# Optimization experiments

Hardware: AMD Instinct MI355X
Metric: run time of the kernel (lower is better)

Reference implementation:

```python
import jax, jax.numpy as jnp
import numpy as np

B, N, C = 4, 2304, 256
H = 8                      # num_heads
D = C // H                 # head_dim = 32
SCALE = D ** -0.5
H_DS, W_DS = 48, 48
UP = 2                     # spatial_down_ratio
EPS = 1e-5


def setup_inputs() -> dict:
    key = jax.random.key(0)
    ks = jax.random.split(key, 16)
    g = lambda k, shape, s: (jax.random.normal(k, shape, dtype=jnp.float32) * s)
    return {
        "x1": g(ks[0], (B, N, C), 1.0),
        "x2": g(ks[1], (B, N, C), 1.0),
        # attention projections (torch Linear convention: [out, in], no bias)
        "q1_w": g(ks[2], (C, C), C ** -0.5),
        "kv1_w": g(ks[3], (2 * C, C), C ** -0.5),
        "q2_w": g(ks[4], (C, C), C ** -0.5),
        "kv2_w": g(ks[5], (2 * C, C), C ** -0.5),
        # per-head scalar biases
        "beta12": jnp.full((H,), 0.2, dtype=jnp.float32),
        "beta21": jnp.full((H,), 0.1, dtype=jnp.float32),
        # output projections
        "p1_w": g(ks[6], (C, C), (2.0 / C) ** 0.5),
        "p1_b": g(ks[7], (C,), 1e-2),
        "p2_w": g(ks[8], (C, C), (2.0 / C) ** 0.5),
        "p2_b": g(ks[9], (C,), 1e-2),
        # LayerNorm affine params
        "g1": jnp.ones((C,), dtype=jnp.float32),
        "b1": jnp.zeros((C,), dtype=jnp.float32),
        "g2": jnp.ones((C,), dtype=jnp.float32),
        "b2": jnp.zeros((C,), dtype=jnp.float32),
    }


def _heads(x):
    # [B,N,C] -> [B,H,N,D]
    return x.reshape(B, N, H, D).transpose(0, 2, 1, 3)


def _merge(x):
    # [B,H,N,D] -> [B,N,C]
    return x.transpose(0, 2, 1, 3).reshape(B, N, C)


def _cross_attn(q, k, v, beta):
    # scores: [B,H,N,N] with per-head scalar bias
    s = jnp.einsum("bhqd,bhkd->bhqk", q, k) * SCALE + beta[None, :, None, None]
    a = jax.nn.softmax(s, axis=-1)
    return jnp.einsum("bhqk,bhkd->bhqd", a, v)


def _layernorm(x, g, b):
    mu = jnp.mean(x, axis=-1, keepdims=True)
    var = jnp.var(x, axis=-1, keepdims=True)
    return (x - mu) * jax.lax.rsqrt(var + EPS) * g + b


def _forward(x1, x2, q1_w, kv1_w, q2_w, kv2_w, beta12, beta21,
             p1_w, p1_b, p2_w, p2_b, g1, b1, g2, b2):
    q1 = _heads(x1 @ q1_w.T)
    kv1 = x1 @ kv1_w.T          # [B,N,2C]
    k1, v1 = _heads(kv1[..., :C]), _heads(kv1[..., C:])
    q2 = _heads(x2 @ q2_w.T)
    kv2 = x2 @ kv2_w.T
    k2, v2 = _heads(kv2[..., :C]), _heads(kv2[..., C:])

    o1 = _merge(_cross_attn(q1, k2, v2, beta12))   # x1 attends to x2
    o2 = _merge(_cross_attn(q2, k1, v1, beta21))   # x2 attends to x1

    y1 = _layernorm(jax.nn.relu(o1 @ p1_w.T + p1_b), g1, b1)
    y2 = _layernorm(jax.nn.relu(o2 @ p2_w.T + p2_b), g2, b2)

    # [B,N,C] -> [B,C,H_ds,W_ds]
    y1 = y1.transpose(0, 2, 1).reshape(B, C, H_DS, W_DS)
    y2 = y2.transpose(0, 2, 1).reshape(B, C, H_DS, W_DS)

    # bilinear upsample x2, align_corners=False (half-pixel == jax.image default)
    out_shape = (B, C, H_DS * UP, W_DS * UP)
    y1 = jax.image.resize(y1, out_shape, method="bilinear")
    y2 = jax.image.resize(y2, out_shape, method="bilinear")
    return y1, y2


def reference(x1, x2, q1_w, kv1_w, q2_w, kv2_w, beta12, beta21,
              p1_w, p1_b, p2_w, p2_b, g1, b1, g2, b2):
    return _forward(x1, x2, q1_w, kv1_w, q2_w, kv2_w, beta12, beta21,
                    p1_w, p1_b, p2_w, p2_b, g1, b1, g2, b2)
```

## Files before the change

kernel.cpp:

```cpp
#include <hip/hip_runtime.h>
#include <math.h>


typedef __attribute__((ext_vector_type(8))) short short8;
typedef __attribute__((ext_vector_type(4))) float f32x4;
typedef __attribute__((ext_vector_type(16))) float f32x16;
typedef __attribute__((ext_vector_type(2))) unsigned uint32x2;

#define MFMA16(a, b, c) __builtin_amdgcn_mfma_f32_16x16x32_bf16((a), (b), (c), 0, 0, 0)
#define MFMA32(a, b, c) __builtin_amdgcn_mfma_f32_32x32x16_bf16((a), (b), (c), 0, 0, 0)

__device__ __forceinline__ float bf2f(ushort u) {
    union { unsigned u; float f; } x; x.u = ((unsigned)u) << 16; return x.f;
}
__device__ __forceinline__ ushort f2bf(float f) {
    union { float f; unsigned u; } x; x.f = f;
    unsigned u = x.u;
    return (ushort)((u + 0x7fffu + ((u >> 16) & 1u)) >> 16);
}
__device__ __forceinline__ unsigned cvt_pk_bf16(float a, float b) {
    unsigned r;
    asm("v_cvt_pk_bf16_f32 %0, %1, %2" : "=v"(r) : "v"(a), "v"(b));
    return r;
}
__device__ __forceinline__ float fast_ex2(float x) {
    float r;
    asm("v_exp_f32 %0, %1" : "=v"(r) : "v"(x));
    return r;
}
__device__ __forceinline__ void plswap(unsigned &a, unsigned &b) {
    uint32x2 r = __builtin_amdgcn_permlane32_swap(a, b, false, false);
    a = r[0]; b = r[1];
}

__global__ void sniff_kernel(const ushort* __restrict__ x, int* __restrict__ flag)
{
    int lane = threadIdx.x;
    ushort u = x[lane * 2];
    int e = (u >> 7) & 0xFF;
    int outlier = (e < 100 || e > 135) ? 1 : 0;
    unsigned long long m = __ballot(outlier);
    if (lane == 0) *flag = (__popcll(m) >= 16) ? 1 : 0;
}

__global__ __launch_bounds__(256) void convert_params(
    const void* s0, const void* s1, const void* s2, const void* s3,
    const void* s4, const void* s5, const void* s6, const void* s7,
    const void* s8, const void* s9, const void* s10, const void* s11,
    ushort* __restrict__ dst, const int* __restrict__ flag)
{
    int idx = blockIdx.x * 256 + threadIdx.x;
    if (idx >= 525824) return;
    const void* src; int off;
    if      (idx < 65536)  { src = s0;  off = idx; }
    else if (idx < 196608) { src = s1;  off = idx - 65536; }
    else if (idx < 262144) { src = s2;  off = idx - 196608; }
    else if (idx < 393216) { src = s3;  off = idx - 262144; }
    else if (idx < 458752) { src = s4;  off = idx - 393216; }
    else if (idx < 524288) { src = s5;  off = idx - 458752; }
    else if (idx < 524544) { src = s6;  off = idx - 524288; }
    else if (idx < 524800) { src = s7;  off = idx - 524544; }
    else if (idx < 525056) { src = s8;  off = idx - 524800; }
    else if (idx < 525312) { src = s9;  off = idx - 525056; }
    else if (idx < 525568) { src = s10; off = idx - 525312; }
    else                   { src = s11; off = idx - 525568; }
    ushort v = (*flag) ? f2bf(((const float*)src)[off])
                       : ((const ushort*)src)[off];
    dst[idx] = v;
}

__global__ __launch_bounds__(256) void convert_x(
    const void* __restrict__ x1, const void* __restrict__ x2,
    ushort* __restrict__ o1, ushort* __restrict__ o2,
    const int* __restrict__ flag)
{
    int idx = blockIdx.x * 256 + threadIdx.x;
    int which = idx >= 294912;
    int off = (which ? idx - 294912 : idx) * 8;
    const void* src = which ? x2 : x1;
    ushort* dst = which ? o2 : o1;
    if (*flag) {
        const float* p = (const float*)src + off;
        float4 a = *(const float4*)p;
        float4 c = *(const float4*)(p + 4);
        uint4 u;
        u.x = cvt_pk_bf16(a.x, a.y);
        u.y = cvt_pk_bf16(a.z, a.w);
        u.z = cvt_pk_bf16(c.x, c.y);
        u.w = cvt_pk_bf16(c.z, c.w);
        *(uint4*)(dst + off) = u;
    } else {
        *(uint4*)(dst + off) = *(const uint4*)((const ushort*)src + off);
    }
}

__global__ __launch_bounds__(256) void gemm_bt(
    const void* __restrict__ Ain, const ushort* __restrict__ W,
    ushort* __restrict__ C, const ushort* __restrict__ bias,
    int M, int N, int K, int relu, const int* __restrict__ dflag, int a_ext,
    int mode, ushort* __restrict__ Kh, ushort* __restrict__ Vt,
    const ushort* __restrict__ W2, const ushort* __restrict__ bias2,
    ushort* __restrict__ Kh2, ushort* __restrict__ Vt2, int mhalf)
{
    __shared__ __align__(16) ushort As[128][40];
    __shared__ __align__(16) ushort Ws[128][40];

    const int m0 = blockIdx.x * 128;
    const int n0 = blockIdx.y * 128;
    const int tid = threadIdx.x;
    const int w = tid >> 6;
    const int wr = w >> 1, wc = w & 1;
    const int lane = tid & 63;
    const int lm = lane & 15;
    const int quad = lane >> 4;
    const int a32 = a_ext ? *dflag : 0;

    const int side = (mhalf && m0 >= mhalf) ? 1 : 0;
    const ushort* Wu = side ? W2 : W;
    const ushort* bu = side ? bias2 : bias;
    ushort* Khu = side ? Kh2 : Kh;
    ushort* Vtu = side ? Vt2 : Vt;

    const f32x4 Z4 = {0.f, 0.f, 0.f, 0.f};
    f32x4 acc[4][4];
    for (int i = 0; i < 4; i++)
        for (int j = 0; j < 4; j++) acc[i][j] = Z4;

    const ushort* A16 = (const ushort*)Ain;
    const float*  A32 = (const float*)Ain;
    const int row = tid >> 1, off16 = (tid & 1) * 16;

    for (int k0 = 0; k0 < K; k0 += 32) {
        __syncthreads();
        if (a32) {
            const float* p0 = A32 + (size_t)(m0 + row) * K + k0 + off16;
            float4 f0 = *(const float4*)p0;
            float4 f1 = *(const float4*)(p0 + 4);
            float4 f2 = *(const float4*)(p0 + 8);
            float4 f3 = *(const float4*)(p0 + 12);
            uint4 t0, t1;
            t0.x = cvt_pk_bf16(f0.x, f0.y);
            t0.y = cvt_pk_bf16(f0.z, f0.w);
            t0.z = cvt_pk_bf16(f1.x, f1.y);
            t0.w = cvt_pk_bf16(f1.z, f1.w);
            t1.x = cvt_pk_bf16(f2.x, f2.y);
            t1.y = cvt_pk_bf16(f2.z, f2.w);
            t1.z = cvt_pk_bf16(f3.x, f3.y);
            t1.w = cvt_pk_bf16(f3.z, f3.w);
            *(uint4*)&As[row][off16]     = t0;
            *(uint4*)&As[row][off16 + 8] = t1;
        } else {
            const ushort* p0 = A16 + (size_t)(m0 + row) * K + k0 + off16;
            *(uint4*)&As[row][off16]     = *(const uint4*)p0;
            *(uint4*)&As[row][off16 + 8] = *(const uint4*)(p0 + 8);
        }
        {
            const ushort* p0 = Wu + (size_t)(n0 + row) * K + k0 + off16;
            *(uint4*)&Ws[row][off16]     = *(const uint4*)p0;
            *(uint4*)&Ws[row][off16 + 8] = *(const uint4*)(p0 + 8);
        }
        __syncthreads();

        short8 af[4], wf[4];
        #pragma unroll
        for (int mt = 0; mt < 4; mt++)
            af[mt] = *(const short8*)&As[wr * 64 + mt * 16 + lm][quad * 8];
        #pragma unroll
        for (int nt = 0; nt < 4; nt++)
            wf[nt] = *(const short8*)&Ws[wc * 64 + nt * 16 + lm][quad * 8];
        #pragma unroll
        for (int mt = 0; mt < 4; mt++)
            #pragma unroll
            for (int nt = 0; nt < 4; nt++)
                acc[mt][nt] = MFMA16(af[mt], wf[nt], acc[mt][nt]);
    }

    if (mode == 1) {
        const float QSC = 0.17677669529663687f * 1.4426950408889634f;
        #pragma unroll
        for (int mt = 0; mt < 4; mt++) {
            const int grow = m0 + wr * 64 + mt * 16 + quad * 4;
            const int grel = grow - (side ? mhalf : 0);
            int bb = grel / 2304;
            int tok = grel - bb * 2304;
            #pragma unroll
            for (int nt = 0; nt < 4; nt++) {
                int col = n0 + wc * 64 + nt * 16 + lm;
                if (col < 256) {
                    for (int r = 0; r < 4; r++)
                        C[(size_t)(grow + r) * 256 + col] = f2bf(acc[mt][nt][r] * QSC);
                } else if (col < 512) {
                    int c2 = col - 256, hh = c2 >> 5, d = c2 & 31;
                    size_t kb = ((size_t)(bb * 8 + hh) * 72 + (tok >> 5)) * 1024
                              + (size_t)(d >> 4) * 512 + (size_t)(d & 15);
                    for (int r = 0; r < 4; r++)
                        Khu[kb + (size_t)((tok + r) & 31) * 16] = f2bf(acc[mt][nt][r]);
                } else {
                    int c2 = col - 512, hh = c2 >> 5, d = c2 & 31;
                    size_t vb = ((size_t)(bb * 8 + hh) * 144 + (tok >> 4)) * 512
                              + (size_t)d * 16 + (size_t)(tok & 15);
                    uint2 o;
                    o.x = cvt_pk_bf16(acc[mt][nt][0], acc[mt][nt][1]);
                    o.y = cvt_pk_bf16(acc[mt][nt][2], acc[mt][nt][3]);
                    *(uint2*)&Vtu[vb] = o;
                }
            }
        }
    } else {
        #pragma unroll
        for (int mt = 0; mt < 4; mt++) {
            const int grow = m0 + wr * 64 + mt * 16 + quad * 4;
            #pragma unroll
            for (int nt = 0; nt < 4; nt++) {
                int col = n0 + wc * 64 + nt * 16 + lm;
                float bv = bu ? bf2f(bu[col]) : 0.f;
                for (int r = 0; r < 4; r++) {
                    float v = acc[mt][nt][r] + bv;
                    if (relu) v = fmaxf(v, 0.f);
                    C[(size_t)(grow + r) * N + col] = f2bf(v);
                }
            }
        }
    }
}

__global__ __launch_bounds__(256) void attn_kernel(
    const ushort* __restrict__ Qa, const ushort* __restrict__ Kha,
    const ushort* __restrict__ Vta, ushort* __restrict__ Oa,
    const ushort* __restrict__ Qb, const ushort* __restrict__ Khb2,
    const ushort* __restrict__ Vtb2, ushort* __restrict__ Ob)
{
    __shared__ float Lo[4][2][64][16];
    __shared__ float Ll[4][2][64];

    const int sid = blockIdx.x;
    const int qb = blockIdx.y;
    const int side = sid >> 5;
    const int bh = sid & 31;
    const ushort* Q  = side ? Qb   : Qa;
    const ushort* Kh = side ? Khb2 : Kha;
    const ushort* Vt = side ? Vtb2 : Vta;
    ushort* O        = side ? Ob   : Oa;

    const int b = bh >> 3, h = bh & 7;
    const int tid = threadIdx.x;
    const int w = tid >> 6, lane = tid & 63;
    const int l31 = lane & 31, hl = lane >> 5;

    const int qrow0 = qb * 64 + l31;
    const int qrow1 = qrow0 + 32;
    const ushort* qp0 = Q + ((size_t)b * 2304 + qrow0) * 256 + h * 32 + hl * 8;
    const ushort* qp1 = Q + ((size_t)b * 2304 + qrow1) * 256 + h * 32 + hl * 8;
    const short8 qf0a = *(const short8*)qp0;
    const short8 qf1a = *(const short8*)(qp0 + 16);
    const short8 qf0b = *(const short8*)qp1;
    const short8 qf1b = *(const short8*)(qp1 + 16);

    f32x16 oa, ob;
    #pragma unroll
    for (int i = 0; i < 16; i++) { oa[i] = 0.f; ob[i] = 0.f; }
    const f32x16 Z16 = oa;
    float la = 0.f, lb = 0.f;

    const ushort* kp0 = Kh + (size_t)bh * 73728 + l31 * 16 + hl * 8;
    const ushort* vp0 = Vt + (size_t)bh * 73728 + l31 * 16 + hl * 8;

#define LOADT(kf0v, kf1v, vf0v, vf1v, t) { \
    const ushort* _kp = kp0 + (size_t)(t) * 1024; \
    kf0v = *(const short8*)_kp; \
    kf1v = *(const short8*)(_kp + 512); \
    const ushort* _vp = vp0 + (size_t)(t) * 1024; \
    vf0v = *(const short8*)_vp; \
    vf1v = *(const short8*)(_vp + 512); \
}
#define QSET(kf0v, kf1v, vf0v, vf1v, qf0v, qf1v, oacc, lacc) { \
    f32x16 s = MFMA32(kf0v, qf0v, Z16); \
    s = MFMA32(kf1v, qf1v, s); \
    float p[16]; \
    _Pragma("unroll") \
    for (int i = 0; i < 16; i++) p[i] = fast_ex2(s[i]); \
    lacc += (((p[0] + p[1]) + (p[2] + p[3])) + ((p[4] + p[5]) + (p[6] + p[7]))) \
          + (((p[8] + p[9]) + (p[10] + p[11])) + ((p[12] + p[13]) + (p[14] + p[15]))); \
    unsigned c0 = cvt_pk_bf16(p[0],  p[1]); \
    unsigned c1 = cvt_pk_bf16(p[2],  p[3]); \
    unsigned c2 = cvt_pk_bf16(p[4],  p[5]); \
    unsigned c3 = cvt_pk_bf16(p[6],  p[7]); \
    unsigned c4 = cvt_pk_bf16(p[8],  p[9]); \
    unsigned c5 = cvt_pk_bf16(p[10], p[11]); \
    unsigned c6 = cvt_pk_bf16(p[12], p[13]); \
    unsigned c7 = cvt_pk_bf16(p[14], p[15]); \
    plswap(c0, c2); plswap(c1, c3); plswap(c4, c6); plswap(c5, c7); \
    union { unsigned u[4]; short8 s8; } pA, pB; \
    pA.u[0] = c0; pA.u[1] = c1; pA.u[2] = c2; pA.u[3] = c3; \
    pB.u[0] = c4; pB.u[1] = c5; pB.u[2] = c6; pB.u[3] = c7; \
    oacc = MFMA32(vf0v, pA.s8, oacc); \
    oacc = MFMA32(vf1v, pB.s8, oacc); \
}
#define COMP(kf0v, kf1v, vf0v, vf1v) { \
    QSET(kf0v, kf1v, vf0v, vf1v, qf0a, qf1a, oa, la); \
    QSET(kf0v, kf1v, vf0v, vf1v, qf0b, qf1b, ob, lb); \
}

    short8 kA0, kA1, vA0, vA1;
    short8 kB0, kB1, vB0, vB1;

    const int t0 = w * 18;

    LOADT(kA0, kA1, vA0, vA1, t0);
    LOADT(kB0, kB1, vB0, vB1, t0 + 1);

    for (int i = 0; i < 9; i++) {
        COMP(kA0, kA1, vA0, vA1);
        { int ta = t0 + 2 * i + 2; ta = ta < 72 ? ta : 70;
          LOADT(kA0, kA1, vA0, vA1, ta); }
        COMP(kB0, kB1, vB0, vB1);
        { int tb = t0 + 2 * i + 3; tb = tb < 72 ? tb : 71;
          LOADT(kB0, kB1, vB0, vB1, tb); }
    }
#undef LOADT
#undef QSET
#undef COMP

    la += __shfl_xor(la, 32, 64);
    lb += __shfl_xor(lb, 32, 64);

    #pragma unroll
    for (int r = 0; r < 16; r++) {
        Lo[w][0][lane][r] = oa[r];
        Lo[w][1][lane][r] = ob[r];
    }
    Ll[w][0][lane] = la;
    Ll[w][1][lane] = lb;
    __syncthreads();

    if (w < 2) {
        float os[16];
        #pragma unroll
        for (int r = 0; r < 16; r++) os[r] = 0.f;
        float ls = 0.f;
        #pragma unroll
        for (int u = 0; u < 4; u++) {
            ls += Ll[u][w][lane];
            #pragma unroll
            for (int r = 0; r < 16; r++) os[r] += Lo[u][w][lane][r];
        }
        float rl = 1.f / ls;
        const int qrow = (w == 0) ? qrow0 : qrow1;
        ushort* op = O + ((size_t)b * 2304 + qrow) * 256 + h * 32 + hl * 4;
        #pragma unroll
        for (int g = 0; g < 4; g++) {
            uint2 o;
            o.x = cvt_pk_bf16(os[4 * g] * rl, os[4 * g + 1] * rl);
            o.y = cvt_pk_bf16(os[4 * g + 2] * rl, os[4 * g + 3] * rl);
            *(uint2*)(op + 8 * g) = o;
        }
    }
}

__global__ __launch_bounds__(256) void lnt_kernel(
    const ushort* __restrict__ Z, const ushort* __restrict__ G1,
    const ushort* __restrict__ B1, const ushort* __restrict__ G2,
    const ushort* __restrict__ B2, ushort* __restrict__ Yt)
{
    __shared__ ushort T[256][72];

    const int tid = threadIdx.x;
    const int tok0 = blockIdx.x * 32;
    const int half = (tok0 >= 9216) ? 1 : 0;
    const int tr = tok0 - half * 9216;
    const int bb = tr / 2304;
    const int tokb = tr - bb * 2304;

    const int tok_l = tid >> 3;
    const int cq = tid & 7;

    const ushort* zp = Z + ((size_t)(tok0 + tok_l)) * 256 + cq * 32;
    uint dd[16];
    for (int i = 0; i < 4; i++) {
        uint4 v = *(const uint4*)(zp + i * 8);
        dd[i * 4 + 0] = v.x; dd[i * 4 + 1] = v.y;
        dd[i * 4 + 2] = v.z; dd[i * 4 + 3] = v.w;
    }
    float s = 0.f, q = 0.f;
    for (int e = 0; e < 16; e++) {
        float x0 = bf2f((ushort)dd[e]);
        float x1 = bf2f((ushort)(dd[e] >> 16));
        s += x0 + x1;
        q += x0 * x0 + x1 * x1;
    }
    s += __shfl_xor(s, 1, 64); q += __shfl_xor(q, 1, 64);
    s += __shfl_xor(s, 2, 64); q += __shfl_xor(q, 2, 64);
    s += __shfl_xor(s, 4, 64); q += __shfl_xor(q, 4, 64);
    float mu = s * (1.f / 256.f);
    float var = q * (1.f / 256.f) - mu * mu;
    float rs = rsqrtf(var + 1e-5f);

    const ushort* Gs = half ? G2 : G1;
    const ushort* Bs = half ? B2 : B1;
    const int col = tok_l + 4 * cq;

    for (int i = 0; i < 4; i++) {
        int cb = cq * 32 + i * 8;
        uint4 gv = *(const uint4*)(Gs + cb);
        uint4 bv = *(const uint4*)(Bs + cb);
        uint gg[4] = {gv.x, gv.y, gv.z, gv.w};
        uint bw[4] = {bv.x, bv.y, bv.z, bv.w};
        for (int k = 0; k < 4; k++) {
            uint u = dd[i * 4 + k];
            float x0 = bf2f((ushort)u), x1 = bf2f((ushort)(u >> 16));
            float y0 = (x0 - mu) * rs * bf2f((ushort)gg[k]) + bf2f((ushort)bw[k]);
            float y1 = (x1 - mu) * rs * bf2f((ushort)(gg[k] >> 16))
                     + bf2f((ushort)(bw[k] >> 16));
            int c = cb + 2 * k;
            T[c][col]     = f2bf(y0);
            T[c + 1][col] = f2bf(y1);
        }
    }
    __syncthreads();

    const int c_row = tid >> 3;
    const int tq = (tid & 7) * 4;
    const size_t obase = ((size_t)((half * 4 + bb) * 256)) * 2304 + tokb + tq;
    for (int i = 0; i < 8; i++) {
        int c = c_row + 32 * i;
        uint2 v = *(const uint2*)&T[c][tq + 4 * i];
        *(uint2*)(Yt + obase + (size_t)c * 2304) = v;
    }
}

__global__ __launch_bounds__(256) void upsample_kernel(
    const ushort* __restrict__ Yt, float* __restrict__ out)
{
    int idx = blockIdx.x * 256 + threadIdx.x;
    int m  = idx % 48;
    int t  = idx / 48;
    int oi = t % 96;
    int bc = t / 96;

    float fi = oi * 0.5f - 0.25f;
    int i0 = (int)floorf(fi);
    float wi = fi - (float)i0;
    int i1 = i0 + 1 < 47 ? i0 + 1 : 47;
    i0 = i0 > 0 ? i0 : 0;
    int jm = m - 1 > 0 ? m - 1 : 0;
    int jp = m + 1 < 47 ? m + 1 : 47;

    const ushort* r0 = Yt + (size_t)bc * 2304 + i0 * 48;
    const ushort* r1 = Yt + (size_t)bc * 2304 + i1 * 48;
    float a0 = bf2f(r0[jm]), b0 = bf2f(r0[m]), c0 = bf2f(r0[jp]);
    float a1 = bf2f(r1[jm]), b1 = bf2f(r1[m]), c1 = bf2f(r1[jp]);
    float u = 1.f - wi;
    float ha = u * a0 + wi * a1;
    float hb = u * b0 + wi * b1;
    float hc = u * c0 + wi * c1;
    float2 o;
    o.x = 0.25f * ha + 0.75f * hb;
    o.y = 0.75f * hb + 0.25f * hc;
    *(float2*)(out + (size_t)bc * 9216 + oi * 96 + m * 2) = o;
}

extern "C" void kernel_launch(void* const* d_in, const int* in_sizes, int n_in,
                              void* d_out, int out_size, void* d_ws, size_t ws_size,
                              hipStream_t stream)
{
    (void)in_sizes; (void)n_in; (void)out_size; (void)ws_size;

    ushort* ws  = (ushort*)d_ws;
    ushort* Q1  = ws;
    ushort* Q2  = Q1  + 2359296;
    ushort* KV1 = Q2  + 2359296;
    ushort* KV2 = KV1 + 4718592;
    ushort* wc  = KV2 + 4718592;
    int*    dflag = (int*)(wc + 525824);

    ushort* cqkv1w = wc;
    ushort* cqkv2w = wc + 196608;
    ushort* cp1w  = wc + 393216;
    ushort* cp2w  = wc + 458752;
    ushort* cp1b  = wc + 524288;
    ushort* cp2b  = wc + 524544;
    ushort* cg1   = wc + 524800;
    ushort* cb1   = wc + 525056;
    ushort* cg2   = wc + 525312;
    ushort* cb2   = wc + 525568;

    float*  outf = (float*)d_out;
    ushort* O1  = (ushort*)d_out;
    ushort* O2  = O1 + 2359296;
    ushort* Xb1 = O2 + 2359296;
    ushort* Xb2 = Xb1 + 2359296;
    ushort* Z1  = KV2;
    ushort* Yt  = Q1;
    (void)Q2; (void)O2; (void)Xb2;

    dim3 blk(256);
    sniff_kernel<<<dim3(1), dim3(64), 0, stream>>>((const ushort*)d_in[0], dflag);
    convert_params<<<dim3(2054), blk, 0, stream>>>(
        d_in[2], d_in[3], d_in[4], d_in[5], d_in[8], d_in[10],
        d_in[9], d_in[11], d_in[12], d_in[13], d_in[14], d_in[15],
        wc, dflag);
    convert_x<<<dim3(2304), blk, 0, stream>>>(d_in[0], d_in[1], Xb1, Xb2, dflag);

    gemm_bt<<<dim3(144, 6), blk, 0, stream>>>(Xb1, cqkv1w, Q1, nullptr,
        18432, 768, 256, 0, dflag, 0, 1, KV1, KV1 + 2359296,
        cqkv2w, nullptr, KV2, KV2 + 2359296, 9216);

    attn_kernel<<<dim3(64, 36), dim3(256), 0, stream>>>(
        Q1, KV2, KV2 + 2359296, O1,
        Q2, KV1, KV1 + 2359296, O2);

    gemm_bt<<<dim3(144, 2), blk, 0, stream>>>(O1, cp1w, Z1, cp1b,
        18432, 256, 256, 1, dflag, 0, 0, nullptr, nullptr,
        cp2w, cp2b, nullptr, nullptr, 9216);

    lnt_kernel<<<dim3(576), blk, 0, stream>>>(Z1, cg1, cb1, cg2, cb2, Yt);

    upsample_kernel<<<dim3(36864), blk, 0, stream>>>(Yt, outf);
}
```

Baseline: 249.6 us.

## Fuse output projection with LayerNorm-transpose and merge prep kernels

Replaces the separate output-projection GEMM and the LayerNorm/transpose kernel with a single kernel that computes 64 full-width rows per block, applies bias+ReLU, reduces row statistics across waves via shared memory, normalizes, and writes the transposed layout directly. It also merges the dtype-sniff, parameter conversion and input conversion into one launch, with every block recomputing the sniff flag. The aim is to remove the intermediate Z round trip through global memory and several launch overheads. In exchange the fused GEMM uses fewer blocks (288) with unpipelined loads, and the dflag passed to gemm_bt becomes null.

```diff
diff --git a/kernel.cpp b/kernel.cpp
--- a/kernel.cpp
+++ b/kernel.cpp
@@ -33,64 +33,61 @@
     a = r[0]; b = r[1];
 }
 
-__global__ void sniff_kernel(const ushort* __restrict__ x, int* __restrict__ flag)
-{
-    int lane = threadIdx.x;
-    ushort u = x[lane * 2];
-    int e = (u >> 7) & 0xFF;
-    int outlier = (e < 100 || e > 135) ? 1 : 0;
-    unsigned long long m = __ballot(outlier);
-    if (lane == 0) *flag = (__popcll(m) >= 16) ? 1 : 0;
-}
-
-__global__ __launch_bounds__(256) void convert_params(
+__global__ __launch_bounds__(256) void prep_kernel(
+    const void* __restrict__ x1, const void* __restrict__ x2,
+    ushort* __restrict__ xo1, ushort* __restrict__ xo2,
     const void* s0, const void* s1, const void* s2, const void* s3,
     const void* s4, const void* s5, const void* s6, const void* s7,
     const void* s8, const void* s9, const void* s10, const void* s11,
-    ushort* __restrict__ dst, const int* __restrict__ flag)
+    ushort* __restrict__ dst)
 {
-    int idx = blockIdx.x * 256 + threadIdx.x;
-    if (idx >= 525824) return;
-    const void* src; int off;
-    if      (idx < 65536)  { src = s0;  off = idx; }
-    else if (idx < 196608) { src = s1;  off = idx - 65536; }
-    else if (idx < 262144) { src = s2;  off = idx - 196608; }
-    else if (idx < 393216) { src = s3;  off = idx - 262144; }
-    else if (idx < 458752) { src = s4;  off = idx - 393216; }
-    else if (idx < 524288) { src = s5;  off = idx - 458752; }
-    else if (idx < 524544) { src = s6;  off = idx - 524288; }
-    else if (idx < 524800) { src = s7;  off = idx - 524544; }
-    else if (idx < 525056) { src = s8;  off = idx - 524800; }
-    else if (idx < 525312) { src = s9;  off = idx - 525056; }
-    else if (idx < 525568) { src = s10; off = idx - 525312; }
-    else                   { src = s11; off = idx - 525568; }
-    ushort v = (*flag) ? f2bf(((const float*)src)[off])
-                       : ((const ushort*)src)[off];
-    dst[idx] = v;
-}
-
-__global__ __launch_bounds__(256) void convert_x(
-    const void* __restrict__ x1, const void* __restrict__ x2,
-    ushort* __restrict__ o1, ushort* __restrict__ o2,
-    const int* __restrict__ flag)
-{
-    int idx = blockIdx.x * 256 + threadIdx.x;
-    int which = idx >= 294912;
-    int off = (which ? idx - 294912 : idx) * 8;
-    const void* src = which ? x2 : x1;
-    ushort* dst = which ? o2 : o1;
-    if (*flag) {
-        const float* p = (const float*)src + off;
-        float4 a = *(const float4*)p;
-        float4 c = *(const float4*)(p + 4);
-        uint4 u;
-        u.x = cvt_pk_bf16(a.x, a.y);
-        u.y = cvt_pk_bf16(a.z, a.w);
-        u.z = cvt_pk_bf16(c.x, c.y);
-        u.w = cvt_pk_bf16(c.z, c.w);
-        *(uint4*)(dst + off) = u;
-    } else {
-        *(uint4*)(dst + off) = *(const uint4*)((const ushort*)src + off);
+    {
+        ushort u = ((const ushort*)x1)[(threadIdx.x & 63) * 2];
+        int e = (u >> 7) & 0xFF;
+        int outlier = (e < 100 || e > 135) ? 1 : 0;
+        unsigned long long mk = __ballot(outlier);
+        int flag = (__popcll(mk) >= 16) ? 1 : 0;
+
+        int bid = blockIdx.x;
+        if (bid < 2304) {
+            int idx = bid * 256 + threadIdx.x;
+            int which = idx >= 294912;
+            int off = (which ? idx - 294912 : idx) * 8;
+            const void* src = which ? x2 : x1;
+            ushort* o = which ? xo2 : xo1;
+            if (flag) {
+                const float* p = (const float*)src + off;
+                float4 a = *(const float4*)p;
+                float4 c = *(const float4*)(p + 4);
+                uint4 u4;
+                u4.x = cvt_pk_bf16(a.x, a.y);
+                u4.y = cvt_pk_bf16(a.z, a.w);
+                u4.z = cvt_pk_bf16(c.x, c.y);
+                u4.w = cvt_pk_bf16(c.z, c.w);
+                *(uint4*)(o + off) = u4;
+            } else {
+                *(uint4*)(o + off) = *(const uint4*)((const ushort*)src + off);
+            }
+        } else {
+            int idx = (bid - 2304) * 256 + threadIdx.x;
+            if (idx >= 525824) return;
+            const void* src; int off;
+            if      (idx < 65536)  { src = s0;  off = idx; }
+            else if (idx < 196608) { src = s1;  off = idx - 65536; }
+            else if (idx < 262144) { src = s2;  off = idx - 196608; }
+            else if (idx < 393216) { src = s3;  off = idx - 262144; }
+            else if (idx < 458752) { src = s4;  off = idx - 393216; }
+            else if (idx < 524288) { src = s5;  off = idx - 458752; }
+            else if (idx < 524544) { src = s6;  off = idx - 524288; }
+            else if (idx < 524800) { src = s7;  off = idx - 524544; }
+            else if (idx < 525056) { src = s8;  off = idx - 524800; }
+            else if (idx < 525312) { src = s9;  off = idx - 525056; }
+            else if (idx < 525568) { src = s10; off = idx - 525312; }
+            else                   { src = s11; off = idx - 525568; }
+            ushort v = flag ? f2bf(((const float*)src)[off])
+                            : ((const ushort*)src)[off];
+            dst[idx] = v;
+        }
     }
 }
 
@@ -357,74 +354,136 @@
     }
 }
 
-__global__ __launch_bounds__(256) void lnt_kernel(
-    const ushort* __restrict__ Z, const ushort* __restrict__ G1,
-    const ushort* __restrict__ B1, const ushort* __restrict__ G2,
-    const ushort* __restrict__ B2, ushort* __restrict__ Yt)
+__global__ __launch_bounds__(256) void projlnt_kernel(
+    const ushort* __restrict__ O,
+    const ushort* __restrict__ W1c, const ushort* __restrict__ b1v,
+    const ushort* __restrict__ g1v, const ushort* __restrict__ t1v,
+    const ushort* __restrict__ W2c, const ushort* __restrict__ b2v,
+    const ushort* __restrict__ g2v, const ushort* __restrict__ t2v,
+    ushort* __restrict__ Yt)
 {
-    __shared__ ushort T[256][72];
+    __shared__ __align__(16) ushort As[64][40];
+    __shared__ __align__(16) ushort Ws[256][40];
+    __shared__ float Sred[4][64][2];
+
+    const int m0 = blockIdx.x * 64;
+    const int side = (m0 >= 9216) ? 1 : 0;
+    const ushort* Wu = side ? W2c : W1c;
+    const ushort* bu = side ? b2v : b1v;
+    const ushort* gu = side ? g2v : g1v;
+    const ushort* tu = side ? t2v : t1v;
 
     const int tid = threadIdx.x;
-    const int tok0 = blockIdx.x * 32;
-    const int half = (tok0 >= 9216) ? 1 : 0;
-    const int tr = tok0 - half * 9216;
-    const int bb = tr / 2304;
-    const int tokb = tr - bb * 2304;
-
-    const int tok_l = tid >> 3;
-    const int cq = tid & 7;
-
-    const ushort* zp = Z + ((size_t)(tok0 + tok_l)) * 256 + cq * 32;
-    uint dd[16];
-    for (int i = 0; i < 4; i++) {
-        uint4 v = *(const uint4*)(zp + i * 8);
-        dd[i * 4 + 0] = v.x; dd[i * 4 + 1] = v.y;
-        dd[i * 4 + 2] = v.z; dd[i * 4 + 3] = v.w;
-    }
-    float s = 0.f, q = 0.f;
-    for (int e = 0; e < 16; e++) {
-        float x0 = bf2f((ushort)dd[e]);
-        float x1 = bf2f((ushort)(dd[e] >> 16));
-        s += x0 + x1;
-        q += x0 * x0 + x1 * x1;
-    }
-    s += __shfl_xor(s, 1, 64); q += __shfl_xor(q, 1, 64);
-    s += __shfl_xor(s, 2, 64); q += __shfl_xor(q, 2, 64);
-    s += __shfl_xor(s, 4, 64); q += __shfl_xor(q, 4, 64);
-    float mu = s * (1.f / 256.f);
-    float var = q * (1.f / 256.f) - mu * mu;
-    float rs = rsqrtf(var + 1e-5f);
-
-    const ushort* Gs = half ? G2 : G1;
-    const ushort* Bs = half ? B2 : B1;
-    const int col = tok_l + 4 * cq;
-
-    for (int i = 0; i < 4; i++) {
-        int cb = cq * 32 + i * 8;
-        uint4 gv = *(const uint4*)(Gs + cb);
-        uint4 bv = *(const uint4*)(Bs + cb);
-        uint gg[4] = {gv.x, gv.y, gv.z, gv.w};
-        uint bw[4] = {bv.x, bv.y, bv.z, bv.w};
-        for (int k = 0; k < 4; k++) {
-            uint u = dd[i * 4 + k];
-            float x0 = bf2f((ushort)u), x1 = bf2f((ushort)(u >> 16));
-            float y0 = (x0 - mu) * rs * bf2f((ushort)gg[k]) + bf2f((ushort)bw[k]);
-            float y1 = (x1 - mu) * rs * bf2f((ushort)(gg[k] >> 16))
-                     + bf2f((ushort)(bw[k] >> 16));
-            int c = cb + 2 * k;
-            T[c][col]     = f2bf(y0);
-            T[c + 1][col] = f2bf(y1);
-        }
+    const int w = tid >> 6, lane = tid & 63;
+    const int lm = lane & 15, quad = lane >> 4;
+
+    const f32x4 Z4 = {0.f, 0.f, 0.f, 0.f};
+    f32x4 acc[4][4];
+    for (int i = 0; i < 4; i++)
+        for (int j = 0; j < 4; j++) acc[i][j] = Z4;
+
+    const int arow = tid >> 2, aoff = (tid & 3) * 8;
+
+    for (int k0 = 0; k0 < 256; k0 += 32) {
+        __syncthreads();
+        *(uint4*)&As[arow][aoff] =
+            *(const uint4*)(O + (size_t)(m0 + arow) * 256 + k0 + aoff);
+        const ushort* wp = Wu + (size_t)tid * 256 + k0;
+        *(uint4*)&Ws[tid][0]  = *(const uint4*)(wp);
+        *(uint4*)&Ws[tid][8]  = *(const uint4*)(wp + 8);
+        *(uint4*)&Ws[tid][16] = *(const uint4*)(wp + 16);
+        *(uint4*)&Ws[tid][24] = *(const uint4*)(wp + 24);
+        __syncthreads();
+
+        short8 af[4], wf[4];
+        #pragma unroll
+        for (int mt = 0; mt < 4; mt++)
+            af[mt] = *(const short8*)&As[mt * 16 + lm][quad * 8];
+        #pragma unroll
+        for (int nt = 0; nt < 4; nt++)
+            wf[nt] = *(const short8*)&Ws[w * 64 + nt * 16 + lm][quad * 8];
+        #pragma unroll
+        for (int mt = 0; mt < 4; mt++)
+            #pragma unroll
+            for (int nt = 0; nt < 4; nt++)
+                acc[mt][nt] = MFMA16(af[mt], wf[nt], acc[mt][nt]);
+    }
+
+    #pragma unroll
+    for (int nt = 0; nt < 4; nt++) {
+        float bv = bf2f(bu[w * 64 + nt * 16 + lm]);
+        #pragma unroll
+        for (int mt = 0; mt < 4; mt++)
+            #pragma unroll
+            for (int r = 0; r < 4; r++)
+                acc[mt][nt][r] = fmaxf(acc[mt][nt][r] + bv, 0.f);
+    }
+
+    float s[4][4], q[4][4];
+    #pragma unroll
+    for (int mt = 0; mt < 4; mt++)
+        #pragma unroll
+        for (int r = 0; r < 4; r++) {
+            float a0 = acc[mt][0][r], a1 = acc[mt][1][r];
+            float a2 = acc[mt][2][r], a3 = acc[mt][3][r];
+            s[mt][r] = (a0 + a1) + (a2 + a3);
+            q[mt][r] = (a0 * a0 + a1 * a1) + (a2 * a2 + a3 * a3);
+        }
+    #pragma unroll
+    for (int off = 1; off < 16; off <<= 1)
+        #pragma unroll
+        for (int mt = 0; mt < 4; mt++)
+            #pragma unroll
+            for (int r = 0; r < 4; r++) {
+                s[mt][r] += __shfl_xor(s[mt][r], off, 64);
+                q[mt][r] += __shfl_xor(q[mt][r], off, 64);
+            }
+    if (lm == 0) {
+        #pragma unroll
+        for (int mt = 0; mt < 4; mt++)
+            #pragma unroll
+            for (int r = 0; r < 4; r++) {
+                int rowl = mt * 16 + quad * 4 + r;
+                Sred[w][rowl][0] = s[mt][r];
+                Sred[w][rowl][1] = q[mt][r];
+            }
     }
     __syncthreads();
 
-    const int c_row = tid >> 3;
-    const int tq = (tid & 7) * 4;
-    const size_t obase = ((size_t)((half * 4 + bb) * 256)) * 2304 + tokb + tq;
-    for (int i = 0; i < 8; i++) {
-        int c = c_row + 32 * i;
-        uint2 v = *(const uint2*)&T[c][tq + 4 * i];
-        *(uint2*)(Yt + obase + (size_t)c * 2304) = v;
+    const int mrel = m0 - side * 9216;
+    const int bb = mrel / 2304;
+    const int tokb = mrel - bb * 2304;
+    #pragma unroll
+    for (int mt = 0; mt < 4; mt++) {
+        float mu[4], rs[4];
+        #pragma unroll
+        for (int r = 0; r < 4; r++) {
+            int rowl = mt * 16 + quad * 4 + r;
+            float S = (Sred[0][rowl][0] + Sred[1][rowl][0])
+                    + (Sred[2][rowl][0] + Sred[3][rowl][0]);
+            float Qq = (Sred[0][rowl][1] + Sred[1][rowl][1])
+                     + (Sred[2][rowl][1] + Sred[3][rowl][1]);
+            float m = S * (1.f / 256.f);
+            float var = Qq * (1.f / 256.f) - m * m;
+            mu[r] = m;
+            rs[r] = rsqrtf(var + 1e-5f);
+        }
+        #pragma unroll
+        for (int nt = 0; nt < 4; nt++) {
+            int col = w * 64 + nt * 16 + lm;
+            float g = bf2f(gu[col]);
+            float bt = bf2f(tu[col]);
+            float y0 = (acc[mt][nt][0] - mu[0]) * rs[0] * g + bt;
+            float y1 = (acc[mt][nt][1] - mu[1]) * rs[1] * g + bt;
+            float y2 = (acc[mt][nt][2] - mu[2]) * rs[2] * g + bt;
+            float y3 = (acc[mt][nt][3] - mu[3]) * rs[3] * g + bt;
+            uint2 o;
+            o.x = cvt_pk_bf16(y0, y1);
+            o.y = cvt_pk_bf16(y2, y3);
+            size_t base = ((size_t)((side * 4 + bb) * 256 + col)) * 2304
+                        + tokb + mt * 16 + quad * 4;
+            *(uint2*)(Yt + base) = o;
+        }
     }
 }
 
@@ -471,7 +530,6 @@
     ushort* KV1 = Q2  + 2359296;
     ushort* KV2 = KV1 + 4718592;
     ushort* wc  = KV2 + 4718592;
-    int*    dflag = (int*)(wc + 525824);
 
     ushort* cqkv1w = wc;
     ushort* cqkv2w = wc + 196608;
@@ -489,31 +547,26 @@
     ushort* O2  = O1 + 2359296;
     ushort* Xb1 = O2 + 2359296;
     ushort* Xb2 = Xb1 + 2359296;
-    ushort* Z1  = KV2;
     ushort* Yt  = Q1;
     (void)Q2; (void)O2; (void)Xb2;
 
     dim3 blk(256);
-    sniff_kernel<<<dim3(1), dim3(64), 0, stream>>>((const ushort*)d_in[0], dflag);
-    convert_params<<<dim3(2054), blk, 0, stream>>>(
+    prep_kernel<<<dim3(4358), blk, 0, stream>>>(
+        d_in[0], d_in[1], Xb1, Xb2,
         d_in[2], d_in[3], d_in[4], d_in[5], d_in[8], d_in[10],
         d_in[9], d_in[11], d_in[12], d_in[13], d_in[14], d_in[15],
-        wc, dflag);
-    convert_x<<<dim3(2304), blk, 0, stream>>>(d_in[0], d_in[1], Xb1, Xb2, dflag);
+        wc);
 
     gemm_bt<<<dim3(144, 6), blk, 0, stream>>>(Xb1, cqkv1w, Q1, nullptr,
-        18432, 768, 256, 0, dflag, 0, 1, KV1, KV1 + 2359296,
+        18432, 768, 256, 0, nullptr, 0, 1, KV1, KV1 + 2359296,
         cqkv2w, nullptr, KV2, KV2 + 2359296, 9216);
 
-    attn_kernel<<<dim3(64, 36), dim3(256), 0, stream>>>(
+    attn_kernel<<<dim3(64, 36), blk, 0, stream>>>(
         Q1, KV2, KV2 + 2359296, O1,
         Q2, KV1, KV1 + 2359296, O2);
 
-    gemm_bt<<<dim3(144, 2), blk, 0, stream>>>(O1, cp1w, Z1, cp1b,
-        18432, 256, 256, 1, dflag, 0, 0, nullptr, nullptr,
-        cp2w, cp2b, nullptr, nullptr, 9216);
-
-    lnt_kernel<<<dim3(576), blk, 0, stream>>>(Z1, cg1, cb1, cg2, cb2, Yt);
+    projlnt_kernel<<<dim3(288), blk, 0, stream>>>(
+        O1, cp1w, cp1b, cg1, cb1, cp2w, cp2b, cg2, cb2, Yt);
 
     upsample_kernel<<<dim3(36864), blk, 0, stream>>>(Yt, outf);
 }
```

Measured after the change: 250.9 us. No clear change (+0.5%).
